# Kernel optimization log

Measured on AMD Instinct MI355X. Metric: run time of the kernel, lower is better.

## Reference

```python
import jax, jax.numpy as jnp
import numpy as np

N = 50000      # num atoms
E = 800000     # num edges
F = 64         # atom_fea_len
NBR = 64       # nbr_fea_len
NCONV = 3
T = 4096       # pooled target atoms
STATE = 2
VOCAB = 100
EPS = 1e-5


def setup_inputs() -> dict:
    key = jax.random.key(0)
    ks = jax.random.split(key, 20)
    Z = 2 * F + NBR  # concat message width
    inp = {
        "x_types": jax.random.randint(ks[0], (N,), 0, VOCAB),
        "edge_index": jax.random.randint(ks[1], (2, E), 0, N),
        "edge_attr": jax.random.normal(ks[2], (E, NBR), dtype=jnp.float32),
        "target": jax.random.randint(ks[3], (T,), 0, N),
        "emb": jax.random.normal(ks[4], (VOCAB, F), dtype=jnp.float32),
        "Wc": jax.random.normal(ks[5], (NCONV, F, Z), dtype=jnp.float32) * 0.05,
        "bc": jnp.zeros((NCONV, F), jnp.float32),
        "Wf": jax.random.normal(ks[6], (NCONV, 1, Z), dtype=jnp.float32) * 0.05,
        "bf": jnp.zeros((NCONV, 1), jnp.float32),
        "g1": jnp.ones((NCONV, F), jnp.float32),
        "b1": jnp.zeros((NCONV, F), jnp.float32),
        "g2": jnp.ones((NCONV, F), jnp.float32),
        "b2": jnp.zeros((NCONV, F), jnp.float32),
        "Wfc": jax.random.normal(ks[7], (F, F), dtype=jnp.float32) * 0.05,
        "bfc": jnp.zeros((F,), jnp.float32),
        "Ws": jax.random.normal(ks[8], (STATE, F), dtype=jnp.float32) * 0.05,
        "bs": jnp.zeros((STATE,), jnp.float32),
    }
    return inp


def _segment_softmax(logits, idx, n):
    # per-target-node softmax over variable-size edge neighborhoods
    m = jax.ops.segment_max(logits, idx, num_segments=n)
    m = jnp.where(jnp.isfinite(m), m, 0.0)
    e = jnp.exp(logits - m[idx])
    s = jax.ops.segment_sum(e, idx, num_segments=n)
    return e / (s[idx] + 1e-16)


def _batchnorm(x, gamma, beta):
    # training-mode BatchNorm1d: biased batch stats over dim 0
    mu = x.mean(0)
    var = x.var(0)
    return (x - mu) * jax.lax.rsqrt(var + EPS) * gamma + beta


def reference(x_types, edge_index, edge_attr, target, emb, Wc, bc, Wf, bf,
              g1, b1, g2, b2, Wfc, bfc, Ws, bs):
    x = emb[x_types]                      # [N, F]
    # flow='target_to_source': i = edge_index[0] (aggregate here), j = edge_index[1]
    idx_i = edge_index[0]
    idx_j = edge_index[1]
    ones = jnp.ones((edge_index.shape[1],), x.dtype)
    cnt = jax.ops.segment_sum(ones, idx_i, num_segments=x.shape[0])
    denom = jnp.maximum(cnt, 1.0)[:, None]
    for l in range(NCONV):
        z = jnp.concatenate([x[idx_i], x[idx_j], edge_attr], axis=1)  # [E, 2F+NBR]
        core = jax.nn.relu(_batchnorm(z @ Wc[l].T + bc[l], g1[l], b1[l]))  # [E, F]
        filt = (z @ Wf[l].T + bf[l])[:, 0]                                  # [E]
        alpha = _segment_softmax(filt, idx_i, x.shape[0])[:, None]          # [E, 1]
        agg = jax.ops.segment_sum(alpha * core, idx_i, num_segments=x.shape[0]) / denom
        x = jax.nn.relu(_batchnorm(agg, g2[l], b2[l]) + x)
    h = jax.nn.relu(x[target])            # [T, F]
    h = jax.nn.relu(h @ Wfc.T + bfc)
    logits = h @ Ws.T + bs                # [T, STATE]
    return jax.nn.softmax(logits, axis=-1)
```

## Files before the change

### kernel.cpp

```cpp
#include <hip/hip_runtime.h>
#include <math.h>

#define N_ATOMS 50000
#define N_EDGES 800000
#define F 64
#define Z 192
#define NCONV 3
#define T_TGT 4096
#define EPS 1e-5f
#define SLOTS 128
#define NB_SCAN 196
#define NBLK_E 2500
#define STEPS_E 5
#define NGRP_N 3125
#define NBLK_N 782

typedef __attribute__((ext_vector_type(4))) float f32x4;
typedef __attribute__((ext_vector_type(8))) short s16x8;
typedef __attribute__((ext_vector_type(8))) __bf16 bf16x8;

static_assert(NBLK_E * 64 * STEPS_E == N_EDGES, "edge tiling exact");

static __device__ __forceinline__ float bf2f(unsigned short u) {
    return __uint_as_float(((unsigned int)u) << 16);
}
static __device__ __forceinline__ unsigned short f2bf(float f) {
    unsigned int u = __float_as_uint(f);
    unsigned int r = u + 0x7FFFu + ((u >> 16) & 1u);
    return (unsigned short)(r >> 16);
}
static __device__ __forceinline__ bf16x8 pack8(float4 a, float4 b) {
    s16x8 r;
    r[0] = (short)f2bf(a.x); r[1] = (short)f2bf(a.y);
    r[2] = (short)f2bf(a.z); r[3] = (short)f2bf(a.w);
    r[4] = (short)f2bf(b.x); r[5] = (short)f2bf(b.y);
    r[6] = (short)f2bf(b.z); r[7] = (short)f2bf(b.w);
    return __builtin_bit_cast(bf16x8, r);
}
static __device__ __forceinline__ uint2 pack4(float a, float b, float c, float d) {
    uint2 r;
    r.x = (unsigned int)f2bf(a) | ((unsigned int)f2bf(b) << 16);
    r.y = (unsigned int)f2bf(c) | ((unsigned int)f2bf(d) << 16);
    return r;
}


__global__ void k_embed(const int* __restrict__ types, const float* __restrict__ emb,
                        float* __restrict__ x, unsigned short* __restrict__ xb) {
    int idx = blockIdx.x * 256 + threadIdx.x;
    if (idx < N_ATOMS * F) {
        int n = idx >> 6, f = idx & 63;
        float v = emb[types[n] * F + f];
        x[idx] = v;
        xb[idx] = f2bf(v);
    }
}

__global__ void k_degree(const int* __restrict__ idx_i, int* __restrict__ cnt) {
    int e = blockIdx.x * 256 + threadIdx.x;
    if (e < N_EDGES) atomicAdd(&cnt[idx_i[e]], 1);
}

__global__ void k_scanA(const int* __restrict__ cnt, int* __restrict__ bsum) {
    __shared__ int s[256];
    int base = blockIdx.x * 256, t = threadIdx.x;
    s[t] = (base + t < N_ATOMS) ? cnt[base + t] : 0;
    __syncthreads();
    for (int o = 128; o > 0; o >>= 1) {
        if (t < o) s[t] += s[t + o];
        __syncthreads();
    }
    if (t == 0) bsum[blockIdx.x] = s[0];
}

__global__ void k_scanB(int* __restrict__ bsum, int* __restrict__ rowptr) {
    __shared__ int s[256];
    int t = threadIdx.x;
    int v = (t < NB_SCAN) ? bsum[t] : 0;
    s[t] = v;
    __syncthreads();
    for (int o = 1; o < 256; o <<= 1) {
        int add = (t >= o) ? s[t - o] : 0;
        __syncthreads();
        s[t] += add;
        __syncthreads();
    }
    if (t < NB_SCAN) bsum[t] = s[t] - v;
    if (t == 0) rowptr[N_ATOMS] = N_EDGES;
}

__global__ void k_scanC(const int* __restrict__ cnt, const int* __restrict__ bsum,
                        int* __restrict__ rowptr) {
    __shared__ int s[256];
    int base = blockIdx.x * 256, t = threadIdx.x;
    int v = (base + t < N_ATOMS) ? cnt[base + t] : 0;
    s[t] = v;
    __syncthreads();
    for (int o = 1; o < 256; o <<= 1) {
        int add = (t >= o) ? s[t - o] : 0;
        __syncthreads();
        s[t] += add;
        __syncthreads();
    }
    if (base + t < N_ATOMS) rowptr[base + t] = bsum[blockIdx.x] + s[t] - v;
}

__global__ void k_scatter(const int* __restrict__ idx_i, const int* __restrict__ idx_j,
                          const int* __restrict__ rowptr, int* __restrict__ wofs,
                          int* __restrict__ i_s, int* __restrict__ j_s,
                          int* __restrict__ einv) {
    int e = blockIdx.x * 256 + threadIdx.x;
    if (e < N_EDGES) {
        int i = idx_i[e];
        int pos = rowptr[i] + atomicAdd(&wofs[i], 1);
        i_s[pos] = i;
        j_s[pos] = idx_j[e];
        einv[e] = pos;
    }
}

__global__ void k_prep2(const float* __restrict__ ea, const int* __restrict__ einv,
                        unsigned short* __restrict__ eab) {
    int idx = blockIdx.x * 256 + threadIdx.x;
    int row = idx >> 3;
    if (row >= N_EDGES) return;
    int seg = (idx & 7) * 8;
    const float* src = ea + (size_t)row * F + seg;
    float4 a = *(const float4*)src;
    float4 b = *(const float4*)(src + 4);
    int pos = einv[row];
    *(bf16x8*)(eab + (size_t)pos * F + seg) = pack8(a, b);
}

__global__ __launch_bounds__(256) void k_node_mm(
    const unsigned short* __restrict__ xb,
    const float* __restrict__ Wc, const float* __restrict__ Wf,
    float* __restrict__ u, unsigned short* __restrict__ v,
    float* __restrict__ pi, float* __restrict__ pj)
{
    __shared__ unsigned short WL[18 * 64 * 8];
    int t = threadIdx.x;
    int lane = t & 63, w = t >> 6;
    int c = lane & 15, g = lane >> 4;
    int goff = g * 8;

    #pragma unroll
    for (int rep = 0; rep < 5; ++rep) {
        int f = rep * 4 + w;
        if (f < 18) {
            int kt = f / 9, m = f % 9;
            bf16x8 val;
            if (m < 8) {
                int colbase = (m < 4) ? 0 : 64;
                const float* wp = Wc + (size_t)((m & 3) * 16 + c) * Z + colbase + kt * 32 + goff;
                val = pack8(*(const float4*)wp, *(const float4*)(wp + 4));
            } else {
                s16x8 zz = {0, 0, 0, 0, 0, 0, 0, 0};
                val = __builtin_bit_cast(bf16x8, zz);
                if (c == 0) {
                    const float* wp = Wf + kt * 32 + goff;
                    val = pack8(*(const float4*)wp, *(const float4*)(wp + 4));
                } else if (c == 1) {
                    const float* wp = Wf + 64 + kt * 32 + goff;
                    val = pack8(*(const float4*)wp, *(const float4*)(wp + 4));
                }
            }
            *(bf16x8*)(WL + ((size_t)f * 64 + lane) * 8) = val;
        }
    }
    __syncthreads();

    int grp = blockIdx.x * 4 + w;
    if (grp >= NGRP_N) return;
    int node = grp * 16 + c;
    const unsigned short* xr = xb + (size_t)node * F;
    bf16x8 X0 = *(const bf16x8*)(xr + goff);
    bf16x8 X1 = *(const bf16x8*)(xr + 32 + goff);

    #define LFR(f) (*(const bf16x8*)(WL + ((size_t)(f) * 64 + lane) * 8))
    f32x4 au[4], av[4], ap = (f32x4){0.f, 0.f, 0.f, 0.f};
    #pragma unroll
    for (int m = 0; m < 4; ++m) {
        au[m] = (f32x4){0.f, 0.f, 0.f, 0.f};
        av[m] = (f32x4){0.f, 0.f, 0.f, 0.f};
        au[m] = __builtin_amdgcn_mfma_f32_16x16x32_bf16(LFR(m), X0, au[m], 0, 0, 0);
        au[m] = __builtin_amdgcn_mfma_f32_16x16x32_bf16(LFR(9 + m), X1, au[m], 0, 0, 0);
        av[m] = __builtin_amdgcn_mfma_f32_16x16x32_bf16(LFR(4 + m), X0, av[m], 0, 0, 0);
        av[m] = __builtin_amdgcn_mfma_f32_16x16x32_bf16(LFR(13 + m), X1, av[m], 0, 0, 0);
    }
    ap = __builtin_amdgcn_mfma_f32_16x16x32_bf16(LFR(8), X0, ap, 0, 0, 0);
    ap = __builtin_amdgcn_mfma_f32_16x16x32_bf16(LFR(17), X1, ap, 0, 0, 0);
    #undef LFR

    float* urow = u + (size_t)node * F + g * 4;
    unsigned short* vrow = v + (size_t)node * F + g * 4;
    #pragma unroll
    for (int m = 0; m < 4; ++m) {
        *(f32x4*)(urow + m * 16) = au[m];
        *(uint2*)(vrow + m * 16) = pack4(av[m][0], av[m][1], av[m][2], av[m][3]);
    }
    if (g == 0) {
        pi[node] = ap[0];
        pj[node] = ap[1];
    }
}

__global__ __launch_bounds__(256) void k_upd_mm(
    const float* __restrict__ agg, const float* __restrict__ bnp,
    const float* __restrict__ g2, const float* __restrict__ b2,
    const float* __restrict__ xin, float* __restrict__ xout,
    const float* __restrict__ Wc, const float* __restrict__ Wf,
    float* __restrict__ u, unsigned short* __restrict__ v,
    float* __restrict__ pi, float* __restrict__ pj)
{
    __shared__ unsigned short WL[18 * 64 * 8];
    __shared__ float bnl[4][64];
    int t = threadIdx.x;
    int lane = t & 63, w = t >> 6;
    int c = lane & 15, g = lane >> 4;
    int goff = g * 8;

    #pragma unroll
    for (int rep = 0; rep < 5; ++rep) {
        int f = rep * 4 + w;
        if (f < 18) {
            int kt = f / 9, m = f % 9;
            bf16x8 val;
            if (m < 8) {
                int colbase = (m < 4) ? 0 : 64;
                const float* wp = Wc + (size_t)((m & 3) * 16 + c) * Z + colbase + kt * 32 + goff;
                val = pack8(*(const float4*)wp, *(const float4*)(wp + 4));
            } else {
                s16x8 zz = {0, 0, 0, 0, 0, 0, 0, 0};
                val = __builtin_bit_cast(bf16x8, zz);
                if (c == 0) {
                    const float* wp = Wf + kt * 32 + goff;
                    val = pack8(*(const float4*)wp, *(const float4*)(wp + 4));
                } else if (c == 1) {
                    const float* wp = Wf + 64 + kt * 32 + goff;
                    val = pack8(*(const float4*)wp, *(const float4*)(wp + 4));
                }
            }
            *(bf16x8*)(WL + ((size_t)f * 64 + lane) * 8) = val;
        }
    }
    if (t < 64) {
        bnl[0][t] = bnp[t];
        bnl[1][t] = bnp[64 + t];
        bnl[2][t] = g2[t];
        bnl[3][t] = b2[t];
    }
    __syncthreads();

    int grp = blockIdx.x * 4 + w;
    if (grp >= NGRP_N) return;
    int node = grp * 16 + c;
    const float* ar = agg + (size_t)node * F;
    const float* xr = xin + (size_t)node * F;

    float xv0[8], xv1[8];
    {
        float4 a0 = *(const float4*)(ar + goff);
        float4 a0b = *(const float4*)(ar + goff + 4);
        float4 a1 = *(const float4*)(ar + 32 + goff);
        float4 a1b = *(const float4*)(ar + 32 + goff + 4);
        float4 x0 = *(const float4*)(xr + goff);
        float4 x0b = *(const float4*)(xr + goff + 4);
        float4 x1 = *(const float4*)(xr + 32 + goff);
        float4 x1b = *(const float4*)(xr + 32 + goff + 4);
        float av0[8] = {a0.x, a0.y, a0.z, a0.w, a0b.x, a0b.y, a0b.z, a0b.w};
        float av1[8] = {a1.x, a1.y, a1.z, a1.w, a1b.x, a1b.y, a1b.z, a1b.w};
        float xw0[8] = {x0.x, x0.y, x0.z, x0.w, x0b.x, x0b.y, x0b.z, x0b.w};
        float xw1[8] = {x1.x, x1.y, x1.z, x1.w, x1b.x, x1b.y, x1b.z, x1b.w};
        #pragma unroll
        for (int q = 0; q < 8; ++q) {
            int f0 = goff + q, f1 = 32 + goff + q;
            xv0[q] = fmaxf((av0[q] - bnl[0][f0]) * bnl[1][f0] * bnl[2][f0] + bnl[3][f0] + xw0[q], 0.f);
            xv1[q] = fmaxf((av1[q] - bnl[0][f1]) * bnl[1][f1] * bnl[2][f1] + bnl[3][f1] + xw1[q], 0.f);
        }
        float4 o;
        o.x = xv0[0]; o.y = xv0[1]; o.z = xv0[2]; o.w = xv0[3];
        *(float4*)(xout + (size_t)node * F + goff) = o;
        o.x = xv0[4]; o.y = xv0[5]; o.z = xv0[6]; o.w = xv0[7];
        *(float4*)(xout + (size_t)node * F + goff + 4) = o;
        o.x = xv1[0]; o.y = xv1[1]; o.z = xv1[2]; o.w = xv1[3];
        *(float4*)(xout + (size_t)node * F + 32 + goff) = o;
        o.x = xv1[4]; o.y = xv1[5]; o.z = xv1[6]; o.w = xv1[7];
        *(float4*)(xout + (size_t)node * F + 32 + goff + 4) = o;
    }
    s16x8 px0, px1;
    #pragma unroll
    for (int q = 0; q < 8; ++q) {
        px0[q] = (short)f2bf(xv0[q]);
        px1[q] = (short)f2bf(xv1[q]);
    }
    bf16x8 X0 = __builtin_bit_cast(bf16x8, px0);
    bf16x8 X1 = __builtin_bit_cast(bf16x8, px1);

    #define LFR(f) (*(const bf16x8*)(WL + ((size_t)(f) * 64 + lane) * 8))
    f32x4 au[4], av[4], ap = (f32x4){0.f, 0.f, 0.f, 0.f};
    #pragma unroll
    for (int m = 0; m < 4; ++m) {
        au[m] = (f32x4){0.f, 0.f, 0.f, 0.f};
        av[m] = (f32x4){0.f, 0.f, 0.f, 0.f};
        au[m] = __builtin_amdgcn_mfma_f32_16x16x32_bf16(LFR(m), X0, au[m], 0, 0, 0);
        au[m] = __builtin_amdgcn_mfma_f32_16x16x32_bf16(LFR(9 + m), X1, au[m], 0, 0, 0);
        av[m] = __builtin_amdgcn_mfma_f32_16x16x32_bf16(LFR(4 + m), X0, av[m], 0, 0, 0);
        av[m] = __builtin_amdgcn_mfma_f32_16x16x32_bf16(LFR(13 + m), X1, av[m], 0, 0, 0);
    }
    ap = __builtin_amdgcn_mfma_f32_16x16x32_bf16(LFR(8), X0, ap, 0, 0, 0);
    ap = __builtin_amdgcn_mfma_f32_16x16x32_bf16(LFR(17), X1, ap, 0, 0, 0);
    #undef LFR

    float* urow = u + (size_t)node * F + g * 4;
    unsigned short* vrow = v + (size_t)node * F + g * 4;
    #pragma unroll
    for (int m = 0; m < 4; ++m) {
        *(f32x4*)(urow + m * 16) = au[m];
        *(uint2*)(vrow + m * 16) = pack4(av[m][0], av[m][1], av[m][2], av[m][3]);
    }
    if (g == 0) {
        pi[node] = ap[0];
        pj[node] = ap[1];
    }
}

__global__ __launch_bounds__(256, 3) void k_edge2(
    const unsigned short* __restrict__ eab,
    const float* __restrict__ u, const unsigned short* __restrict__ v,
    const int* __restrict__ i_s, const int* __restrict__ j_s,
    const float* __restrict__ Wc, const float* __restrict__ Wf,
    const float* __restrict__ pi, const float* __restrict__ pj,
    unsigned short* __restrict__ y, float* __restrict__ filt,
    float* __restrict__ stats)
{
    __shared__ unsigned short WL[10 * 64 * 8];
    int t = threadIdx.x;
    int lane = t & 63, w = t >> 6;
    int c = lane & 15, g = lane >> 4;
    int goff = g * 8;

    #pragma unroll
    for (int rep = 0; rep < 3; ++rep) {
        int f = rep * 4 + w;
        if (f < 10) {
            int kt = f / 5, nt = f % 5;
            bf16x8 val;
            if (nt < 4) {
                const float* wp = Wc + (size_t)(nt * 16 + c) * Z + 128 + kt * 32 + goff;
                val = pack8(*(const float4*)wp, *(const float4*)(wp + 4));
            } else {
                s16x8 zz = {0, 0, 0, 0, 0, 0, 0, 0};
                val = __builtin_bit_cast(bf16x8, zz);
                if (c == 0) {
                    const float* wp = Wf + 128 + kt * 32 + goff;
                    val = pack8(*(const float4*)wp, *(const float4*)(wp + 4));
                }
            }
            *(bf16x8*)(WL + ((size_t)f * 64 + lane) * 8) = val;
        }
    }
    __syncthreads();

    bf16x8 A[2][5];
    #pragma unroll
    for (int kt = 0; kt < 2; ++kt)
        #pragma unroll
        for (int nt = 0; nt < 5; ++nt)
            A[kt][nt] = *(const bf16x8*)(WL + ((size_t)(kt * 5 + nt) * 64 + lane) * 8);

    float ssum[4][4] = {{0.f}}, ssq[4][4] = {{0.f}};

    int e = blockIdx.x * (STEPS_E * 64) + w * 16 + c;
    int ie = i_s[e], je = j_s[e];
    bf16x8 E0 = *(const bf16x8*)(eab + (size_t)e * F + goff);
    bf16x8 E1 = *(const bf16x8*)(eab + (size_t)e * F + 32 + goff);

    for (int s = 0; s < STEPS_E; ++s) {
        const float* ur = u + (size_t)ie * F + g * 4;
        const unsigned short* vr = v + (size_t)je * F + g * 4;
        float4 uu[4];
        uint2 vv[4];
        #pragma unroll
        for (int nt = 0; nt < 4; ++nt) {
            uu[nt] = *(const float4*)(ur + nt * 16);
            vv[nt] = *(const uint2*)(vr + nt * 16);
        }
        float fi = 0.f, fj = 0.f;
        if (g == 0) { fi = pi[ie]; fj = pj[je]; }

        int e2 = e, ie2 = ie, je2 = je;
        bf16x8 E0n = E0, E1n = E1;
        if (s + 1 < STEPS_E) {
            e2 = e + 64;
            ie2 = i_s[e2];
            je2 = j_s[e2];
            E0n = *(const bf16x8*)(eab + (size_t)e2 * F + goff);
            E1n = *(const bf16x8*)(eab + (size_t)e2 * F + 32 + goff);
        }

        f32x4 acc[5];
        #pragma unroll
        for (int nt = 0; nt < 5; ++nt) {
            acc[nt] = (f32x4){0.f, 0.f, 0.f, 0.f};
            acc[nt] = __builtin_amdgcn_mfma_f32_16x16x32_bf16(A[0][nt], E0, acc[nt], 0, 0, 0);
            acc[nt] = __builtin_amdgcn_mfma_f32_16x16x32_bf16(A[1][nt], E1, acc[nt], 0, 0, 0);
        }

        unsigned short* yr = y + (size_t)e * F + g * 4;
        #pragma unroll
        for (int nt = 0; nt < 4; ++nt) {
            float y0 = acc[nt][0] + uu[nt].x + bf2f((unsigned short)(vv[nt].x & 0xffff));
            float y1 = acc[nt][1] + uu[nt].y + bf2f((unsigned short)(vv[nt].x >> 16));
            float y2 = acc[nt][2] + uu[nt].z + bf2f((unsigned short)(vv[nt].y & 0xffff));
            float y3 = acc[nt][3] + uu[nt].w + bf2f((unsigned short)(vv[nt].y >> 16));
            ssum[nt][0] += y0; ssq[nt][0] += y0 * y0;
            ssum[nt][1] += y1; ssq[nt][1] += y1 * y1;
            ssum[nt][2] += y2; ssq[nt][2] += y2 * y2;
            ssum[nt][3] += y3; ssq[nt][3] += y3 * y3;
            *(uint2*)(yr + nt * 16) = pack4(y0, y1, y2, y3);
        }
        if (g == 0) filt[e] = acc[4][0] + fi + fj;

        e = e2; ie = ie2; je = je2; E0 = E0n; E1 = E1n;
    }

    int slot = (blockIdx.x & (SLOTS - 1)) * 128;
    #pragma unroll
    for (int nt = 0; nt < 4; ++nt) {
        #pragma unroll
        for (int q = 0; q < 4; ++q) {
            float S = ssum[nt][q], Q = ssq[nt][q];
            S += __shfl_xor(S, 1, 64); S += __shfl_xor(S, 2, 64);
            S += __shfl_xor(S, 4, 64); S += __shfl_xor(S, 8, 64);
            Q += __shfl_xor(Q, 1, 64); Q += __shfl_xor(Q, 2, 64);
            Q += __shfl_xor(Q, 4, 64); Q += __shfl_xor(Q, 8, 64);
            if (c == 0) {
                int f = nt * 16 + g * 4 + q;
                atomicAdd(&stats[slot + f], S);
                atomicAdd(&stats[slot + 64 + f], Q);
            }
        }
    }
}


__global__ void k_finbn(float* __restrict__ stats, float* __restrict__ bnp, float count) {
    __shared__ float red[4][128];
    int t = threadIdx.x;
    int f = t & 63, grp = t >> 6;
    float S = 0.f, Q = 0.f;
    for (int s = grp; s < SLOTS; s += 4) {
        S += stats[s * 128 + f];
        Q += stats[s * 128 + 64 + f];
    }
    red[grp][f] = S;
    red[grp][64 + f] = Q;
    __syncthreads();
    for (int i = t; i < SLOTS * 128; i += 256) stats[i] = 0.f;
    if (t < 64) {
        float Sa = red[0][t] + red[1][t] + red[2][t] + red[3][t];
        float Qa = red[0][64 + t] + red[1][64 + t] + red[2][64 + t] + red[3][64 + t];
        float mu = Sa / count;
        float var = fmaxf(Qa / count - mu * mu, 0.f);
        bnp[t] = mu;
        bnp[64 + t] = 1.f / sqrtf(var + EPS);
    }
}

__global__ __launch_bounds__(256) void k_node_agg(
    const unsigned short* __restrict__ y, const float* __restrict__ filt,
    const int* __restrict__ rowptr, const int* __restrict__ cnt,
    const float* __restrict__ bnp, const float* __restrict__ g1, const float* __restrict__ b1,
    float* __restrict__ agg, float* __restrict__ stats)
{
    __shared__ float sbuf[4][64];
    int t = threadIdx.x;
    int lane = t & 63, wv = t >> 6;
    int node = blockIdx.x * 4 + wv;
    int beg = rowptr[node], end = rowptr[node + 1];
    int es = lane >> 4, fq = lane & 15;
    float4 mu4 = *(const float4*)(bnp + fq * 4);
    float4 rs4 = *(const float4*)(bnp + 64 + fq * 4);
    float4 ga4 = *(const float4*)(g1 + fq * 4);
    float4 be4 = *(const float4*)(b1 + fq * 4);

    float fm = -INFINITY;
    for (int i = beg + lane; i < end; i += 64) fm = fmaxf(fm, filt[i]);
    #pragma unroll
    for (int o = 32; o > 0; o >>= 1) fm = fmaxf(fm, __shfl_xor(fm, o, 64));

    float a0 = 0.f, a1 = 0.f, a2 = 0.f, a3 = 0.f, ss = 0.f;
    #pragma unroll 2
    for (int base = beg; base < end; base += 4) {
        int ee = base + es;
        int eec = min(ee, end - 1);
        float wgt = (ee < end) ? expf(filt[eec] - fm) : 0.f;
        ushort4 yv = *(const ushort4*)(y + (size_t)eec * F + fq * 4);
        float c0 = fmaxf((bf2f(yv.x) - mu4.x) * rs4.x * ga4.x + be4.x, 0.f);
        float c1 = fmaxf((bf2f(yv.y) - mu4.y) * rs4.y * ga4.y + be4.y, 0.f);
        float c2 = fmaxf((bf2f(yv.z) - mu4.z) * rs4.z * ga4.z + be4.z, 0.f);
        float c3 = fmaxf((bf2f(yv.w) - mu4.w) * rs4.w * ga4.w + be4.w, 0.f);
        a0 += wgt * c0; a1 += wgt * c1; a2 += wgt * c2; a3 += wgt * c3;
        ss += wgt;
    }
    #pragma unroll
    for (int o = 16; o <= 32; o <<= 1) {
        a0 += __shfl_xor(a0, o, 64);
        a1 += __shfl_xor(a1, o, 64);
        a2 += __shfl_xor(a2, o, 64);
        a3 += __shfl_xor(a3, o, 64);
        ss += __shfl_xor(ss, o, 64);
    }
    float dn = fmaxf((float)cnt[node], 1.f);
    float inv = 1.f / ((ss + 1e-16f) * dn);
    float o0 = a0 * inv, o1 = a1 * inv, o2 = a2 * inv, o3 = a3 * inv;
    if (lane < 16) {
        float4 o4;
        o4.x = o0; o4.y = o1; o4.z = o2; o4.w = o3;
        *(float4*)(agg + (size_t)node * F + fq * 4) = o4;
        sbuf[wv][fq * 4 + 0] = o0;
        sbuf[wv][fq * 4 + 1] = o1;
        sbuf[wv][fq * 4 + 2] = o2;
        sbuf[wv][fq * 4 + 3] = o3;
    }
    __syncthreads();
    int slot = (blockIdx.x & (SLOTS - 1)) * 128;
    if (t < 64) {
        float s2 = sbuf[0][t] + sbuf[1][t] + sbuf[2][t] + sbuf[3][t];
        atomicAdd(&stats[slot + t], s2);
    }
    __syncthreads();
    if (lane < 16) {
        sbuf[wv][fq * 4 + 0] = o0 * o0;
        sbuf[wv][fq * 4 + 1] = o1 * o1;
        sbuf[wv][fq * 4 + 2] = o2 * o2;
        sbuf[wv][fq * 4 + 3] = o3 * o3;
    }
    __syncthreads();
    if (t < 64) {
        float q2 = sbuf[0][t] + sbuf[1][t] + sbuf[2][t] + sbuf[3][t];
        atomicAdd(&stats[slot + 64 + t], q2);
    }
}

__global__ void k_node_upd(const float* __restrict__ agg, const float* __restrict__ bnp,
                           const float* __restrict__ g2, const float* __restrict__ b2,
                           const float* __restrict__ xin, float* __restrict__ xout) {
    int idx = blockIdx.x * 256 + threadIdx.x;
    if (idx < N_ATOMS * F) {
        int f = idx & 63;
        float v = (agg[idx] - bnp[f]) * bnp[64 + f] * g2[f] + b2[f] + xin[idx];
        xout[idx] = fmaxf(v, 0.f);
    }
}


__global__ __launch_bounds__(256) void k_head(
    const float* __restrict__ x, const int* __restrict__ target,
    const float* __restrict__ Wfc, const float* __restrict__ bfc,
    const float* __restrict__ Ws, const float* __restrict__ bs,
    float* __restrict__ out)
{
    __shared__ float hbuf[4][64];
    int t = threadIdx.x;
    int lane = t & 63, w = t >> 6;
    int tt = blockIdx.x * 4 + w;
    int a = target[min(tt, T_TGT - 1)];
    float h = fmaxf(x[(size_t)a * F + lane], 0.f);
    hbuf[w][lane] = h;
    __syncthreads();
    float acc = bfc[lane];
    #pragma unroll 8
    for (int k = 0; k < F; ++k) acc += hbuf[w][k] * Wfc[lane * F + k];
    float h2 = fmaxf(acc, 0.f);
    float p0 = h2 * Ws[lane];
    float p1 = h2 * Ws[F + lane];
    #pragma unroll
    for (int o = 32; o > 0; o >>= 1) {
        p0 += __shfl_xor(p0, o, 64);
        p1 += __shfl_xor(p1, o, 64);
    }
    if (lane == 0 && tt < T_TGT) {
        float l0 = p0 + bs[0], l1 = p1 + bs[1];
        float mx = fmaxf(l0, l1);
        float e0v = expf(l0 - mx), e1v = expf(l1 - mx);
        float inv = 1.f / (e0v + e1v);
        out[tt * 2 + 0] = e0v * inv;
        out[tt * 2 + 1] = e1v * inv;
    }
}


extern "C" void kernel_launch(void* const* d_in, const int* in_sizes, int n_in,
                              void* d_out, int out_size, void* d_ws, size_t ws_size,
                              hipStream_t stream)
{
    const int*   x_types = (const int*)d_in[0];
    const int*   eidx    = (const int*)d_in[1];
    const float* ea      = (const float*)d_in[2];
    const int*   target  = (const int*)d_in[3];
    const float* emb     = (const float*)d_in[4];
    const float* Wc      = (const float*)d_in[5];
    const float* Wf      = (const float*)d_in[7];
    const float* g1      = (const float*)d_in[9];
    const float* b1      = (const float*)d_in[10];
    const float* g2      = (const float*)d_in[11];
    const float* b2      = (const float*)d_in[12];
    const float* Wfc     = (const float*)d_in[13];
    const float* bfc     = (const float*)d_in[14];
    const float* Ws      = (const float*)d_in[15];
    const float* bs      = (const float*)d_in[16];
    float* out = (float*)d_out;
    const int* idx_i = eidx;
    const int* idx_j = eidx + N_EDGES;

    char* p = (char*)d_ws;
    auto alloc = [&](size_t bytes) {
        char* r = p;
        p += (bytes + 255) & ~(size_t)255;
        return r;
    };
    float* xa            = (float*)alloc((size_t)N_ATOMS * F * 4);
    float* xb_f          = (float*)alloc((size_t)N_ATOMS * F * 4);
    unsigned short* x16a = (unsigned short*)alloc((size_t)N_ATOMS * F * 2);
    unsigned short* eab  = (unsigned short*)alloc((size_t)N_EDGES * F * 2);
    unsigned short* ybuf = (unsigned short*)alloc((size_t)N_EDGES * F * 2);
    float* filt          = (float*)alloc((size_t)N_EDGES * 4);
    float* ubuf          = (float*)alloc((size_t)N_ATOMS * F * 4);
    unsigned short* vbuf = (unsigned short*)alloc((size_t)N_ATOMS * F * 2);
    float* pi            = (float*)alloc((size_t)N_ATOMS * 4);
    float* pj            = (float*)alloc((size_t)N_ATOMS * 4);
    float* agg           = (float*)alloc((size_t)N_ATOMS * F * 4);
    int* cnt             = (int*)alloc((size_t)N_ATOMS * 4);
    int* rowptr          = (int*)alloc((size_t)(N_ATOMS + 1) * 4);
    int* wofs            = (int*)alloc((size_t)N_ATOMS * 4);
    int* i_s             = (int*)alloc((size_t)N_EDGES * 4);
    int* j_s             = (int*)alloc((size_t)N_EDGES * 4);
    int* einv            = (int*)alloc((size_t)N_EDGES * 4);
    int* bsum            = (int*)alloc(256 * 4);
    float* stats         = (float*)alloc((size_t)SLOTS * 128 * 4);
    float* bnp1          = (float*)alloc(128 * 4);
    float* bnp2          = (float*)alloc(128 * 4);
    (void)ws_size; (void)in_sizes; (void)n_in; (void)out_size;

    hipMemsetAsync(cnt, 0, (size_t)N_ATOMS * 4, stream);
    hipMemsetAsync(wofs, 0, (size_t)N_ATOMS * 4, stream);
    hipMemsetAsync(stats, 0, (size_t)SLOTS * 128 * 4, stream);
    k_embed<<<(N_ATOMS * F + 255) / 256, 256, 0, stream>>>(x_types, emb, xa, x16a);
    k_degree<<<(N_EDGES + 255) / 256, 256, 0, stream>>>(idx_i, cnt);
    k_scanA<<<NB_SCAN, 256, 0, stream>>>(cnt, bsum);
    k_scanB<<<1, 256, 0, stream>>>(bsum, rowptr);
    k_scanC<<<NB_SCAN, 256, 0, stream>>>(cnt, bsum, rowptr);
    k_scatter<<<(N_EDGES + 255) / 256, 256, 0, stream>>>(idx_i, idx_j, rowptr, wofs,
                                                         i_s, j_s, einv);
    k_prep2<<<(N_EDGES * 8) / 256, 256, 0, stream>>>(ea, einv, eab);

    float* xcur = xa;
    float* xnxt = xb_f;
    for (int l = 0; l < NCONV; ++l) {
        if (l == 0) {
            k_node_mm<<<NBLK_N, 256, 0, stream>>>(x16a,
                Wc, Wf, ubuf, vbuf, pi, pj);
        } else {
            k_upd_mm<<<NBLK_N, 256, 0, stream>>>(
                agg, bnp2, g2 + (size_t)(l - 1) * F, b2 + (size_t)(l - 1) * F,
                xcur, xnxt,
                Wc + (size_t)l * F * Z, Wf + (size_t)l * Z,
                ubuf, vbuf, pi, pj);
            float* tf = xcur; xcur = xnxt; xnxt = tf;
        }
        k_edge2<<<NBLK_E, 256, 0, stream>>>(
            eab, ubuf, vbuf, i_s, j_s,
            Wc + (size_t)l * F * Z, Wf + (size_t)l * Z,
            pi, pj,
            ybuf, filt, stats);
        k_finbn<<<1, 256, 0, stream>>>(stats, bnp1, (float)N_EDGES);
        k_node_agg<<<N_ATOMS / 4, 256, 0, stream>>>(ybuf, filt, rowptr, cnt, bnp1,
                                                    g1 + (size_t)l * F, b1 + (size_t)l * F,
                                                    agg, stats);
        k_finbn<<<1, 256, 0, stream>>>(stats, bnp2, (float)N_ATOMS);
    }
    k_node_upd<<<(N_ATOMS * F + 255) / 256, 256, 0, stream>>>(
        agg, bnp2, g2 + (size_t)(NCONV - 1) * F, b2 + (size_t)(NCONV - 1) * F,
        xcur, xnxt);
    k_head<<<T_TGT / 4, 256, 0, stream>>>(xnxt, target, Wfc, bfc, Ws, bs, out);
}
```

Baseline: 697.0 us.

## Split BN statistics out of edge kernel to raise its occupancy

```diff
diff --git a/kernel.cpp b/kernel.cpp
--- a/kernel.cpp
+++ b/kernel.cpp
@@ -12,6 +12,7 @@
 #define NB_SCAN 196
 #define NBLK_E 2500
 #define STEPS_E 5
+#define NBLK_YS 1024
 #define NGRP_N 3125
 #define NBLK_N 782
 
@@ -20,6 +21,7 @@
 typedef __attribute__((ext_vector_type(8))) __bf16 bf16x8;
 
 static_assert(NBLK_E * 64 * STEPS_E == N_EDGES, "edge tiling exact");
+static_assert((NBLK_YS * 256) % 8 == 0, "ystats stride multiple of 8");
 
 static __device__ __forceinline__ float bf2f(unsigned short u) {
     return __uint_as_float(((unsigned int)u) << 16);
@@ -325,14 +327,13 @@
     }
 }
 
-__global__ __launch_bounds__(256, 3) void k_edge2(
+__global__ __launch_bounds__(256, 8) void k_edge2(
     const unsigned short* __restrict__ eab,
     const float* __restrict__ u, const unsigned short* __restrict__ v,
     const int* __restrict__ i_s, const int* __restrict__ j_s,
     const float* __restrict__ Wc, const float* __restrict__ Wf,
     const float* __restrict__ pi, const float* __restrict__ pj,
-    unsigned short* __restrict__ y, float* __restrict__ filt,
-    float* __restrict__ stats)
+    unsigned short* __restrict__ y, float* __restrict__ filt)
 {
     __shared__ unsigned short WL[10 * 64 * 8];
     int t = threadIdx.x;
@@ -362,14 +363,7 @@
     }
     __syncthreads();
 
-    bf16x8 A[2][5];
-    #pragma unroll
-    for (int kt = 0; kt < 2; ++kt)
-        #pragma unroll
-        for (int nt = 0; nt < 5; ++nt)
-            A[kt][nt] = *(const bf16x8*)(WL + ((size_t)(kt * 5 + nt) * 64 + lane) * 8);
-
-    float ssum[4][4] = {{0.f}}, ssq[4][4] = {{0.f}};
+    #define AFR(kt, nt) (*(const bf16x8*)(WL + ((size_t)((kt) * 5 + (nt)) * 64 + lane) * 8))
 
     int e = blockIdx.x * (STEPS_E * 64) + w * 16 + c;
     int ie = i_s[e], je = j_s[e];
@@ -403,8 +397,8 @@
         #pragma unroll
         for (int nt = 0; nt < 5; ++nt) {
             acc[nt] = (f32x4){0.f, 0.f, 0.f, 0.f};
-            acc[nt] = __builtin_amdgcn_mfma_f32_16x16x32_bf16(A[0][nt], E0, acc[nt], 0, 0, 0);
-            acc[nt] = __builtin_amdgcn_mfma_f32_16x16x32_bf16(A[1][nt], E1, acc[nt], 0, 0, 0);
+            acc[nt] = __builtin_amdgcn_mfma_f32_16x16x32_bf16(AFR(0, nt), E0, acc[nt], 0, 0, 0);
+            acc[nt] = __builtin_amdgcn_mfma_f32_16x16x32_bf16(AFR(1, nt), E1, acc[nt], 0, 0, 0);
         }
 
         unsigned short* yr = y + (size_t)e * F + g * 4;
@@ -414,33 +408,55 @@
             float y1 = acc[nt][1] + uu[nt].y + bf2f((unsigned short)(vv[nt].x >> 16));
             float y2 = acc[nt][2] + uu[nt].z + bf2f((unsigned short)(vv[nt].y & 0xffff));
             float y3 = acc[nt][3] + uu[nt].w + bf2f((unsigned short)(vv[nt].y >> 16));
-            ssum[nt][0] += y0; ssq[nt][0] += y0 * y0;
-            ssum[nt][1] += y1; ssq[nt][1] += y1 * y1;
-            ssum[nt][2] += y2; ssq[nt][2] += y2 * y2;
-            ssum[nt][3] += y3; ssq[nt][3] += y3 * y3;
             *(uint2*)(yr + nt * 16) = pack4(y0, y1, y2, y3);
         }
         if (g == 0) filt[e] = acc[4][0] + fi + fj;
 
         e = e2; ie = ie2; je = je2; E0 = E0n; E1 = E1n;
     }
-
+    #undef AFR
+}
+
+__global__ __launch_bounds__(256) void k_ystats(const unsigned short* __restrict__ y,
+                                                float* __restrict__ stats) {
+    __shared__ float sb[4][128];
+    int t = threadIdx.x;
+    int lane = t & 63, wv = t >> 6;
+    float s[8] = {0.f, 0.f, 0.f, 0.f, 0.f, 0.f, 0.f, 0.f};
+    float q[8] = {0.f, 0.f, 0.f, 0.f, 0.f, 0.f, 0.f, 0.f};
+    const long long nchunk = (long long)N_EDGES * 8;
+    long long stride = (long long)NBLK_YS * 256;
+    for (long long k = (long long)blockIdx.x * 256 + t; k < nchunk; k += stride) {
+        bf16x8 ch = *(const bf16x8*)(y + k * 8);
+        s16x8 bits = __builtin_bit_cast(s16x8, ch);
+        #pragma unroll
+        for (int j = 0; j < 8; ++j) {
+            float vv = bf2f((unsigned short)bits[j]);
+            s[j] += vv;
+            q[j] += vv * vv;
+        }
+    }
+    #pragma unroll
+    for (int j = 0; j < 8; ++j) {
+        #pragma unroll
+        for (int o = 8; o <= 32; o <<= 1) {
+            s[j] += __shfl_xor(s[j], o, 64);
+            q[j] += __shfl_xor(q[j], o, 64);
+        }
+    }
+    int oct = lane & 7;
+    if (lane < 8) {
+        #pragma unroll
+        for (int j = 0; j < 8; ++j) {
+            sb[wv][oct * 8 + j] = s[j];
+            sb[wv][64 + oct * 8 + j] = q[j];
+        }
+    }
+    __syncthreads();
     int slot = (blockIdx.x & (SLOTS - 1)) * 128;
-    #pragma unroll
-    for (int nt = 0; nt < 4; ++nt) {
-        #pragma unroll
-        for (int q = 0; q < 4; ++q) {
-            float S = ssum[nt][q], Q = ssq[nt][q];
-            S += __shfl_xor(S, 1, 64); S += __shfl_xor(S, 2, 64);
-            S += __shfl_xor(S, 4, 64); S += __shfl_xor(S, 8, 64);
-            Q += __shfl_xor(Q, 1, 64); Q += __shfl_xor(Q, 2, 64);
-            Q += __shfl_xor(Q, 4, 64); Q += __shfl_xor(Q, 8, 64);
-            if (c == 0) {
-                int f = nt * 16 + g * 4 + q;
-                atomicAdd(&stats[slot + f], S);
-                atomicAdd(&stats[slot + 64 + f], Q);
-            }
-        }
+    if (t < 128) {
+        float val = sb[0][t] + sb[1][t] + sb[2][t] + sb[3][t];
+        atomicAdd(&stats[slot + t], val);
     }
 }
 
@@ -674,7 +690,8 @@
             eab, ubuf, vbuf, i_s, j_s,
             Wc + (size_t)l * F * Z, Wf + (size_t)l * Z,
             pi, pj,
-            ybuf, filt, stats);
+            ybuf, filt);
+        k_ystats<<<NBLK_YS, 256, 0, stream>>>(ybuf, stats);
         k_finbn<<<1, 256, 0, stream>>>(stats, bnp1, (float)N_EDGES);
         k_node_agg<<<N_ATOMS / 4, 256, 0, stream>>>(ybuf, filt, rowptr, cnt, bnp1,
                                                     g1 + (size_t)l * F, b1 + (size_t)l * F,
```

Measured after the change: 816.7 us. +17.2%, slower.
